# Performance work log

Hardware: AMD Instinct MI355X
Metric: run time of the kernel (lower is better)

Reference implementation:

```python
import jax, jax.numpy as jnp
import numpy as np

EPS = 1e-12      # F.normalize eps
LN_EPS = 1e-5    # nn.LayerNorm eps
SLOPE = 0.01     # LeakyReLU negative slope
SCALE = 5.0      # attention temperature used by the module


def _l2norm(x):
    n = jnp.sqrt(jnp.sum(x * x, axis=-1, keepdims=True))
    return x / jnp.maximum(n, EPS)


def _layer_norm(x, g, b):
    m = jnp.mean(x, axis=-1, keepdims=True)
    v = jnp.mean((x - m) ** 2, axis=-1, keepdims=True)
    return (x - m) / jnp.sqrt(v + LN_EPS) * g + b


def _leaky(x):
    return jnp.where(x >= 0, x, SLOPE * x)


def setup_inputs() -> dict:
    key = jax.random.key(0)
    ks = jax.random.split(key, 18)
    B, T, N, C = 8, 8, 25, 256
    n = T * N  # 200 == num_nodes
    inp = {
        "local_feat": jax.random.normal(ks[0], (B, T, N, C), dtype=jnp.float32),
        "global_feat": jax.random.normal(ks[1], (B, C), dtype=jnp.float32),
        "pos": jax.random.uniform(ks[2], (B, T, N, 9), dtype=jnp.float32),
        # Diff_prop params
        "dp_adj_w": jax.random.normal(ks[3], (C, C), dtype=jnp.float32) / np.sqrt(C),
        "dp_aff_w": jax.random.normal(ks[4], (C, C), dtype=jnp.float32) * np.sqrt(2.0 / C),
        "dp_aff_b": jnp.zeros((C,), dtype=jnp.float32),
        "dp_ln_g": jnp.ones((C,), dtype=jnp.float32),
        "dp_ln_b": jnp.zeros((C,), dtype=jnp.float32),
        # Feat_aggr params
        "fa_adj_w": jax.random.normal(ks[5], (C, C), dtype=jnp.float32) / np.sqrt(C),
        "fa_aff_w": jax.random.normal(ks[6], (C, C), dtype=jnp.float32) * np.sqrt(2.0 / C),
        "fa_aff_b": jnp.zeros((C,), dtype=jnp.float32),
        "fa_ln_g": jnp.ones((C,), dtype=jnp.float32),
        "fa_ln_b": jnp.zeros((C,), dtype=jnp.float32),
        # Node_att params (Linear(num_nodes+9, 1): weight [1, n+9])
        "na_w": jax.random.normal(ks[7], (1, n + 9), dtype=jnp.float32) * np.sqrt(2.0 / (n + 9)),
        "na_b": jnp.zeros((1,), dtype=jnp.float32),
    }
    return inp


def _diff_prop(lf4, adj_w, aff_w, aff_b, ln_g, ln_b):
    B, T, N, C = lf4.shape
    n = T * N
    lf = lf4.reshape(B, n, C)
    nf = _l2norm(lf)
    # quadratic-form attention: A[b,i,j] = nf_i W nf_j
    A = jnp.einsum('bnc,cd,bmd->bnm', nf, adj_w, nf)
    A = jnp.exp(SCALE * (A - jnp.max(A, axis=-1, keepdims=True)))
    A = A * (1.0 - jnp.eye(n, dtype=A.dtype))
    A = A / jnp.maximum(jnp.sum(A, axis=-1, keepdims=True), EPS)  # L1 row norm (A>=0)
    # full pairwise difference tensor [B, n, n, C]
    diff = lf[:, :, None, :] - lf[:, None, :, :]
    diff = jnp.einsum('bijc,dc->bijd', diff, aff_w) + aff_b
    agg = jnp.einsum('bij,bijd->bid', A, diff)
    out = _leaky(_layer_norm(agg, ln_g, ln_b))
    return out.reshape(B, T, N, C)


def _feat_aggr(lf4, adj_w, aff_w, aff_b, ln_g, ln_b):
    B, T, N, C = lf4.shape
    n = T * N
    lf = lf4.reshape(B, n, C)
    nf = _l2norm(lf)
    A = jnp.einsum('bnc,cd,bmd->bnm', nf, adj_w, nf)
    A = jax.nn.softmax(SCALE * (A - jnp.max(A, axis=-1, keepdims=True)), axis=-1)
    lf = jnp.einsum('bnc,dc->bnd', lf, aff_w) + aff_b
    lf = jnp.einsum('bij,bjk->bik', A, lf)
    out = _leaky(_layer_norm(lf, ln_g, ln_b))
    return out.reshape(B, T, N, C)


def _node_att(lf4, pos, w, b):
    B, T, N, C = lf4.shape
    n = T * N
    lf = lf4.reshape(B, n, C)
    p = pos.reshape(B, n, -1)
    nf = _l2norm(lf)
    A = jnp.einsum('bnc,bmc->bnm', nf, nf)            # [B, n, n]
    src = jnp.concatenate([A, p], axis=-1)            # [B, n, n+9]
    att = jax.nn.sigmoid(jnp.einsum('bni,oi->bno', src, w) + b)  # [B, n, 1]
    att = att.reshape(B, T, N, 1)
    return lf4 * att


def reference(local_feat, global_feat, pos,
              dp_adj_w, dp_aff_w, dp_aff_b, dp_ln_g, dp_ln_b,
              fa_adj_w, fa_aff_w, fa_aff_b, fa_ln_g, fa_ln_b,
              na_w, na_b):
    x = _diff_prop(local_feat, dp_adj_w, dp_aff_w, dp_aff_b, dp_ln_g, dp_ln_b)
    x = _feat_aggr(x, fa_adj_w, fa_aff_w, fa_aff_b, fa_ln_g, fa_ln_b)
    x = _node_att(x, pos, na_w, na_b)
    return x
```

## Files before the change

kernel.cpp:

```cpp
#include <hip/hip_runtime.h>
#include <math.h>

#define Bn 8
#define NN 200
#define Cc 256
#define RR (Bn*NN)
#define JP 200
#define N_EPS 1e-12f
#define LN_EPS 1e-5f
#define SLOPE 0.01f
#define SCALE 5.0f

#define FMA4(acc, s, v) { acc.x = fmaf((s), (v).x, acc.x); acc.y = fmaf((s), (v).y, acc.y); \
                          acc.z = fmaf((s), (v).z, acc.z); acc.w = fmaf((s), (v).w, acc.w); }

__device__ __forceinline__ float wave_reduce_sum(float v) {
    #pragma unroll
    for (int o = 32; o > 0; o >>= 1) v += __shfl_xor(v, o);
    return v;
}

__device__ __forceinline__ float2 half_reduce_sum2(float2 v, float* sh, int h) {
    __syncthreads();
    #pragma unroll
    for (int o = 32; o > 0; o >>= 1) { v.x += __shfl_xor(v.x, o); v.y += __shfl_xor(v.y, o); }
    int w = threadIdx.x >> 6;
    if ((threadIdx.x & 63) == 0) { sh[w*2] = v.x; sh[w*2+1] = v.y; }
    __syncthreads();
    int b0 = h * 8;
    return make_float2(sh[b0]+sh[b0+2]+sh[b0+4]+sh[b0+6],
                       sh[b0+1]+sh[b0+3]+sh[b0+5]+sh[b0+7]);
}

__device__ __forceinline__ float2 half_reduce_max2(float2 v, float* sh, int h) {
    __syncthreads();
    #pragma unroll
    for (int o = 32; o > 0; o >>= 1) {
        v.x = fmaxf(v.x, __shfl_xor(v.x, o));
        v.y = fmaxf(v.y, __shfl_xor(v.y, o));
    }
    int w = threadIdx.x >> 6;
    if ((threadIdx.x & 63) == 0) { sh[w*2] = v.x; sh[w*2+1] = v.y; }
    __syncthreads();
    int b0 = h * 8;
    return make_float2(fmaxf(fmaxf(sh[b0],sh[b0+2]), fmaxf(sh[b0+4],sh[b0+6])),
                       fmaxf(fmaxf(sh[b0+1],sh[b0+3]), fmaxf(sh[b0+5],sh[b0+7])));
}

__global__ void k_tr(const float* __restrict__ dp_aff_w, const float* __restrict__ fa_aff_w,
                     float* __restrict__ WT1, float* __restrict__ WT2) {
    __shared__ float tile[32][33];
    int tb = blockIdx.x;
    const float* S; float* D;
    if (tb < 64) { S = dp_aff_w; D = WT1; } else { S = fa_aff_w; D = WT2; tb -= 64; }
    int bx = tb & 7, by = tb >> 3;
    int tx = threadIdx.x & 31, ty = threadIdx.x >> 5;
    #pragma unroll
    for (int k = 0; k < 32; k += 8)
        tile[ty + k][tx] = S[(size_t)(by*32 + ty + k) * Cc + bx*32 + tx];
    __syncthreads();
    #pragma unroll
    for (int k = 0; k < 32; k += 8)
        D[(size_t)(bx*32 + ty + k) * Cc + by*32 + tx] = tile[tx][ty + k];
}

__global__ void k_pre(const float* __restrict__ lf, const float* __restrict__ dp_adj_w,
                      const float* __restrict__ WT1,
                      float* __restrict__ nfT, float* __restrict__ M, float* __restrict__ P) {
    __shared__ __align__(16) float sx[8][Cc];
    __shared__ __align__(16) float buf[8192];
    int bid = blockIdx.x;
    int t = threadIdx.x, lane = t & 63, wvi = t >> 6;
    bool nb = bid < RR/8;
    int r0 = (nb ? bid : bid - RR/8) * 8;
    const float* W = nb ? dp_adj_w : WT1;
    #pragma unroll
    for (int k = 0; k < 2; k++) {
        int r = 2*wvi + k;
        float4 x = ((const float4*)(lf + (size_t)(r0 + r) * Cc))[lane];
        if (nb) {
            float ss = wave_reduce_sum(x.x*x.x + x.y*x.y + x.z*x.z + x.w*x.w);
            float inv = 1.f / fmaxf(sqrtf(ss), N_EPS);
            x.x *= inv; x.y *= inv; x.z *= inv; x.w *= inv;
        }
        ((float4*)&sx[r][0])[lane] = x;
    }
    __syncthreads();
    if (nb) {
        int b = r0 / NN, i0 = r0 % NN;
        float4 cA, cB;
        cA.x = sx[0][t]; cA.y = sx[1][t]; cA.z = sx[2][t]; cA.w = sx[3][t];
        cB.x = sx[4][t]; cB.y = sx[5][t]; cB.z = sx[6][t]; cB.w = sx[7][t];
        float* np = nfT + (size_t)b * Cc * JP + (size_t)t * JP + i0;
        *((float4*)np) = cA;
        *((float4*)(np + 4)) = cB;
    }
    {
        int qc = t & 63, cid = t >> 6;
        int c0 = cid * 64;
        float4 z = make_float4(0.f,0.f,0.f,0.f);
        float4 acc0=z, acc1=z, acc2=z, acc3=z, acc4=z, acc5=z, acc6=z, acc7=z;
        #pragma unroll 4
        for (int c4 = c0; c4 < c0 + 64; c4 += 4) {
            float4 w0 = *(const float4*)(W + (size_t)(c4+0) * Cc + 4*qc);
            float4 w1 = *(const float4*)(W + (size_t)(c4+1) * Cc + 4*qc);
            float4 w2 = *(const float4*)(W + (size_t)(c4+2) * Cc + 4*qc);
            float4 w3 = *(const float4*)(W + (size_t)(c4+3) * Cc + 4*qc);
            float4 xr;
            xr = *(const float4*)(&sx[0][c4]);
            FMA4(acc0, xr.x, w0); FMA4(acc0, xr.y, w1); FMA4(acc0, xr.z, w2); FMA4(acc0, xr.w, w3);
            xr = *(const float4*)(&sx[1][c4]);
            FMA4(acc1, xr.x, w0); FMA4(acc1, xr.y, w1); FMA4(acc1, xr.z, w2); FMA4(acc1, xr.w, w3);
            xr = *(const float4*)(&sx[2][c4]);
            FMA4(acc2, xr.x, w0); FMA4(acc2, xr.y, w1); FMA4(acc2, xr.z, w2); FMA4(acc2, xr.w, w3);
            xr = *(const float4*)(&sx[3][c4]);
            FMA4(acc3, xr.x, w0); FMA4(acc3, xr.y, w1); FMA4(acc3, xr.z, w2); FMA4(acc3, xr.w, w3);
            xr = *(const float4*)(&sx[4][c4]);
            FMA4(acc4, xr.x, w0); FMA4(acc4, xr.y, w1); FMA4(acc4, xr.z, w2); FMA4(acc4, xr.w, w3);
            xr = *(const float4*)(&sx[5][c4]);
            FMA4(acc5, xr.x, w0); FMA4(acc5, xr.y, w1); FMA4(acc5, xr.z, w2); FMA4(acc5, xr.w, w3);
            xr = *(const float4*)(&sx[6][c4]);
            FMA4(acc6, xr.x, w0); FMA4(acc6, xr.y, w1); FMA4(acc6, xr.z, w2); FMA4(acc6, xr.w, w3);
            xr = *(const float4*)(&sx[7][c4]);
            FMA4(acc7, xr.x, w0); FMA4(acc7, xr.y, w1); FMA4(acc7, xr.z, w2); FMA4(acc7, xr.w, w3);
        }
        float4* b4 = (float4*)buf;
        int o = cid * 512 + qc;
        b4[o      ] = acc0; b4[o +  64] = acc1; b4[o + 128] = acc2; b4[o + 192] = acc3;
        b4[o + 256] = acc4; b4[o + 320] = acc5; b4[o + 384] = acc6; b4[o + 448] = acc7;
    }
    __syncthreads();
    {
        float4* b4 = (float4*)buf;
        float* Y = nb ? M : P;
        #pragma unroll
        for (int k = 0; k < 2; k++) {
            int o4 = t + k*256;
            int r = o4 >> 6, qc = o4 & 63;
            float4 s0 = b4[o4], s1 = b4[512 + o4], s2 = b4[1024 + o4], s3 = b4[1536 + o4];
            float4 sv;
            sv.x = (s0.x + s1.x) + (s2.x + s3.x);
            sv.y = (s0.y + s1.y) + (s2.y + s3.y);
            sv.z = (s0.z + s1.z) + (s2.z + s3.z);
            sv.w = (s0.w + s1.w) + (s2.w + s3.w);
            *(float4*)(Y + (size_t)(r0 + r) * Cc + 4*qc) = sv;
        }
    }
}

__global__ void k_row1f(const float* __restrict__ nfT, const float* __restrict__ Min,
                        const float* __restrict__ P, const float* __restrict__ dp_aff_b,
                        const float* __restrict__ g, const float* __restrict__ bb,
                        const float* __restrict__ fa_adj_w, const float* __restrict__ WT2,
                        const float* __restrict__ fa_aff_b,
                        float* __restrict__ nfT2, float* __restrict__ M2,
                        float* __restrict__ lf2) {
    __shared__ __align__(16) float smT[Cc*4];
    __shared__ __align__(16) float saraw[4*NN];
    __shared__ __align__(16) float saT[NN*4];
    __shared__ __align__(16) float suT[Cc*4];
    __shared__ __align__(16) float buf[8192];
    __shared__ float sh[16];
    __shared__ float sinv[4];
    int t = threadIdx.x, h = t >> 8, tt = t & 255;
    int b = blockIdx.x & 7;
    int i0 = (blockIdx.x >> 3) * 4;
    size_t base = (size_t)b * NN * Cc;
    {
        const float* src = Min + base + (size_t)i0 * Cc;
        #pragma unroll
        for (int o = t; o < 1024; o += 512) {
            int c = o >> 2, r = o & 3;
            smT[o] = src[(size_t)r * Cc + c];
        }
    }
    __syncthreads();
    {
        int q = t & 63, cid = t >> 6;
        if (q < 50) {
            int c0 = cid * 32;
            const float* nfp = nfT + (size_t)b * Cc * JP + (size_t)c0 * JP + 4*q;
            float4 z4 = make_float4(0.f,0.f,0.f,0.f);
            float4 a0 = z4, a1 = z4, a2 = z4, a3 = z4;
            #pragma unroll 8
            for (int c = 0; c < 32; c++) {
                float4 v  = *(const float4*)(nfp + (size_t)c * JP);
                float4 mv = *(const float4*)(&smT[(c0 + c) * 4]);
                FMA4(a0, mv.x, v); FMA4(a1, mv.y, v);
                FMA4(a2, mv.z, v); FMA4(a3, mv.w, v);
            }
            float* pp = buf + cid * 800 + 4*q;
            *(float4*)(pp      ) = a0;
            *(float4*)(pp + 200) = a1;
            *(float4*)(pp + 400) = a2;
            *(float4*)(pp + 600) = a3;
        }
    }
    __syncthreads();
    for (int o = t; o < 800; o += 512) {
        float s = 0.f;
        #pragma unroll
        for (int p = 0; p < 8; p++) s += buf[p*800 + o];
        saraw[o] = s;
    }
    __syncthreads();
    int lr0 = h, lr1 = h + 2;
    float2 vm;
    vm.x = (tt < NN) ? saraw[lr0*NN + tt] : -INFINITY;
    vm.y = (tt < NN) ? saraw[lr1*NN + tt] : -INFINITY;
    float2 m = half_reduce_max2(vm, sh, h);
    float e0 = (tt < NN && tt != i0 + lr0) ? expf(SCALE * (vm.x - m.x)) : 0.f;
    float e1 = (tt < NN && tt != i0 + lr1) ? expf(SCALE * (vm.y - m.y)) : 0.f;
    float2 sum = half_reduce_sum2(make_float2(e0, e1), sh, h);
    if (tt < NN) {
        saT[tt*4 + lr0] = e0 / fmaxf(sum.x, N_EPS);
        saT[tt*4 + lr1] = e1 / fmaxf(sum.y, N_EPS);
    }
    float s0 = sum.x / fmaxf(sum.x, N_EPS);
    float s1 = sum.y / fmaxf(sum.y, N_EPS);
    __syncthreads();
    const float* Pb = P + base;
    {
        int qc = t & 63, jc = t >> 6;
        int j0 = jc * 25;
        float4 z4 = make_float4(0.f,0.f,0.f,0.f);
        float4 u0 = z4, u1 = z4, u2 = z4, u3 = z4;
        #pragma unroll 5
        for (int j = j0; j < j0 + 25; j++) {
            float4 pv = *(const float4*)(Pb + (size_t)j * Cc + 4*qc);
            float4 av = *(const float4*)(&saT[j*4]);
            FMA4(u0, av.x, pv); FMA4(u1, av.y, pv);
            FMA4(u2, av.z, pv); FMA4(u3, av.w, pv);
        }
        float* pp = buf + jc*1024 + 4*qc;
        *(float4*)(pp      ) = u0;
        *(float4*)(pp + 256) = u1;
        *(float4*)(pp + 512) = u2;
        *(float4*)(pp + 768) = u3;
    }
    __syncthreads();
    float acc0 = 0.f, acc1 = 0.f;
    #pragma unroll
    for (int p = 0; p < 8; p++) { acc0 += buf[p*1024 + t]; acc1 += buf[p*1024 + t + 512]; }
    float bv = dp_aff_b[tt];
    float y0 = fmaf(s0, Pb[(size_t)(i0 + lr0) * Cc + tt] + bv, -acc0);
    float y1 = fmaf(s1, Pb[(size_t)(i0 + lr1) * Cc + tt] + bv, -acc1);
    float gg = g[tt], bbv = bb[tt];
    float2 mean2 = half_reduce_sum2(make_float2(y0, y1), sh, h);
    float d0 = y0 - mean2.x * (1.f/256.f);
    float d1 = y1 - mean2.y * (1.f/256.f);
    float2 var2 = half_reduce_sum2(make_float2(d0*d0, d1*d1), sh, h);
    float z0 = d0 / sqrtf(var2.x * (1.f/256.f) + LN_EPS) * gg + bbv;
    float z1 = d1 / sqrtf(var2.y * (1.f/256.f) + LN_EPS) * gg + bbv;
    z0 = (z0 >= 0.f) ? z0 : SLOPE * z0;
    z1 = (z1 >= 0.f) ? z1 : SLOPE * z1;
    suT[tt*4 + lr0] = z0; suT[tt*4 + lr1] = z1;
    float2 ss2 = half_reduce_sum2(make_float2(z0*z0, z1*z1), sh, h);
    if (tt == 0) {
        sinv[lr0] = 1.f / fmaxf(sqrtf(ss2.x), N_EPS);
        sinv[lr1] = 1.f / fmaxf(sqrtf(ss2.y), N_EPS);
    }
    __syncthreads();
    if (h == 0) {
        float4 col;
        col.x = suT[tt*4+0] * sinv[0]; col.y = suT[tt*4+1] * sinv[1];
        col.z = suT[tt*4+2] * sinv[2]; col.w = suT[tt*4+3] * sinv[3];
        *((float4*)(nfT2 + (size_t)b * Cc * JP + (size_t)tt * JP + i0)) = col;
    }
    {
        int qc = t & 63, gidx = t >> 6;
        int mt = gidx & 1, cch = gidx >> 1;
        const float* Wm = mt ? WT2 : fa_adj_w;
        int c0 = cch * 64;
        float4 z4 = make_float4(0.f,0.f,0.f,0.f);
        float4 d0v = z4, d1v = z4, d2v = z4, d3v = z4;
        #pragma unroll 8
        for (int c = c0; c < c0 + 64; c++) {
            float4 wv = *(const float4*)(Wm + (size_t)c * Cc + 4*qc);
            float4 uv = *(const float4*)(&suT[c*4]);
            FMA4(d0v, uv.x, wv); FMA4(d1v, uv.y, wv);
            FMA4(d2v, uv.z, wv); FMA4(d3v, uv.w, wv);
        }
        float* pp = buf + cch*2048 + mt*1024 + 4*qc;
        *(float4*)(pp      ) = d0v;
        *(float4*)(pp + 256) = d1v;
        *(float4*)(pp + 512) = d2v;
        *(float4*)(pp + 768) = d3v;
    }
    __syncthreads();
    {
        float4* b4 = (float4*)buf;
        int o4 = t;
        int mt2 = o4 >> 8, r2 = (o4 >> 6) & 3, qc2 = o4 & 63;
        float4 s0 = b4[o4], s1 = b4[512 + o4], s2 = b4[1024 + o4], s3 = b4[1536 + o4];
        float4 sv;
        sv.x = (s0.x + s1.x) + (s2.x + s3.x);
        sv.y = (s0.y + s1.y) + (s2.y + s3.y);
        sv.z = (s0.z + s1.z) + (s2.z + s3.z);
        sv.w = (s0.w + s1.w) + (s2.w + s3.w);
        if (mt2 == 0) {
            float sc = sinv[r2];
            sv.x *= sc; sv.y *= sc; sv.z *= sc; sv.w *= sc;
            *(float4*)(M2 + base + (size_t)(i0 + r2) * Cc + 4*qc2) = sv;
        } else {
            float4 fb = *(const float4*)(fa_aff_b + 4*qc2);
            sv.x += fb.x; sv.y += fb.y; sv.z += fb.z; sv.w += fb.w;
            *(float4*)(lf2 + base + (size_t)(i0 + r2) * Cc + 4*qc2) = sv;
        }
    }
}

__global__ void k_row2f(const float* __restrict__ nfT2, const float* __restrict__ M2,
                        const float* __restrict__ lf2, const float* __restrict__ g,
                        const float* __restrict__ bb, float* __restrict__ x2,
                        float* __restrict__ nf3) {
    __shared__ __align__(16) float smT[Cc*4];
    __shared__ __align__(16) float saraw[4*NN];
    __shared__ __align__(16) float saT[NN*4];
    __shared__ __align__(16) float buf[8192];
    __shared__ float sh[16];
    int t = threadIdx.x, h = t >> 8, tt = t & 255;
    int b = blockIdx.x & 7;
    int i0 = (blockIdx.x >> 3) * 4;
    size_t base = (size_t)b * NN * Cc;
    {
        const float* src = M2 + base + (size_t)i0 * Cc;
        #pragma unroll
        for (int o = t; o < 1024; o += 512) {
            int c = o >> 2, r = o & 3;
            smT[o] = src[(size_t)r * Cc + c];
        }
    }
    __syncthreads();
    {
        int q = t & 63, cid = t >> 6;
        if (q < 50) {
            int c0 = cid * 32;
            const float* nfp = nfT2 + (size_t)b * Cc * JP + (size_t)c0 * JP + 4*q;
            float4 z4 = make_float4(0.f,0.f,0.f,0.f);
            float4 a0 = z4, a1 = z4, a2 = z4, a3 = z4;
            #pragma unroll 8
            for (int c = 0; c < 32; c++) {
                float4 v  = *(const float4*)(nfp + (size_t)c * JP);
                float4 mv = *(const float4*)(&smT[(c0 + c) * 4]);
                FMA4(a0, mv.x, v); FMA4(a1, mv.y, v);
                FMA4(a2, mv.z, v); FMA4(a3, mv.w, v);
            }
            float* pp = buf + cid * 800 + 4*q;
            *(float4*)(pp      ) = a0;
            *(float4*)(pp + 200) = a1;
            *(float4*)(pp + 400) = a2;
            *(float4*)(pp + 600) = a3;
        }
    }
    __syncthreads();
    for (int o = t; o < 800; o += 512) {
        float s = 0.f;
        #pragma unroll
        for (int p = 0; p < 8; p++) s += buf[p*800 + o];
        saraw[o] = s;
    }
    __syncthreads();
    int lr0 = h, lr1 = h + 2;
    float2 vm;
    vm.x = (tt < NN) ? saraw[lr0*NN + tt] : -INFINITY;
    vm.y = (tt < NN) ? saraw[lr1*NN + tt] : -INFINITY;
    float2 m = half_reduce_max2(vm, sh, h);
    float e0 = (tt < NN) ? expf(SCALE * (vm.x - m.x)) : 0.f;
    float e1 = (tt < NN) ? expf(SCALE * (vm.y - m.y)) : 0.f;
    float2 sum = half_reduce_sum2(make_float2(e0, e1), sh, h);
    if (tt < NN) { saT[tt*4 + lr0] = e0 / sum.x; saT[tt*4 + lr1] = e1 / sum.y; }
    __syncthreads();
    const float* l2b = lf2 + base;
    {
        int qc = t & 63, jc = t >> 6;
        int j0 = jc * 25;
        float4 z4 = make_float4(0.f,0.f,0.f,0.f);
        float4 u0 = z4, u1 = z4, u2 = z4, u3 = z4;
        #pragma unroll 5
        for (int j = j0; j < j0 + 25; j++) {
            float4 pv = *(const float4*)(l2b + (size_t)j * Cc + 4*qc);
            float4 av = *(const float4*)(&saT[j*4]);
            FMA4(u0, av.x, pv); FMA4(u1, av.y, pv);
            FMA4(u2, av.z, pv); FMA4(u3, av.w, pv);
        }
        float* pp = buf + jc*1024 + 4*qc;
        *(float4*)(pp      ) = u0;
        *(float4*)(pp + 256) = u1;
        *(float4*)(pp + 512) = u2;
        *(float4*)(pp + 768) = u3;
    }
    __syncthreads();
    float y0 = 0.f, y1 = 0.f;
    #pragma unroll
    for (int p = 0; p < 8; p++) { y0 += buf[p*1024 + t]; y1 += buf[p*1024 + t + 512]; }
    float gg = g[tt], bbv = bb[tt];
    float2 mean2 = half_reduce_sum2(make_float2(y0, y1), sh, h);
    float d0 = y0 - mean2.x * (1.f/256.f);
    float d1 = y1 - mean2.y * (1.f/256.f);
    float2 var2 = half_reduce_sum2(make_float2(d0*d0, d1*d1), sh, h);
    float z0 = d0 / sqrtf(var2.x * (1.f/256.f) + LN_EPS) * gg + bbv;
    float z1 = d1 / sqrtf(var2.y * (1.f/256.f) + LN_EPS) * gg + bbv;
    z0 = (z0 >= 0.f) ? z0 : SLOPE * z0;
    z1 = (z1 >= 0.f) ? z1 : SLOPE * z1;
    x2[base + (size_t)(i0 + lr0) * Cc + tt] = z0;
    x2[base + (size_t)(i0 + lr1) * Cc + tt] = z1;
    float2 ss2 = half_reduce_sum2(make_float2(z0*z0, z1*z1), sh, h);
    nf3[base + (size_t)(i0 + lr0) * Cc + tt] = z0 / fmaxf(sqrtf(ss2.x), N_EPS);
    nf3[base + (size_t)(i0 + lr1) * Cc + tt] = z1 / fmaxf(sqrtf(ss2.y), N_EPS);
}

__global__ void k_natt(const float* __restrict__ x2, const float* __restrict__ nf3,
                       const float* __restrict__ pos, const float* __restrict__ w,
                       const float* __restrict__ nb, float* __restrict__ out) {
    __shared__ float svb[4][Cc];
    int t = threadIdx.x, lane = t & 63, wv = t >> 6;
    int b = blockIdx.x & 7;
    int i = (blockIdx.x >> 3) * 4 + wv;
    const float4* slab = (const float4*)(nf3 + (size_t)b * NN * Cc);
    float4 acc = make_float4(0.f, 0.f, 0.f, 0.f);
    for (int j = wv * 50; j < wv * 50 + 50; j++) {
        float4 q = slab[j * 64 + lane];
        float wj = w[j];
        acc.x = fmaf(wj, q.x, acc.x);
        acc.y = fmaf(wj, q.y, acc.y);
        acc.z = fmaf(wj, q.z, acc.z);
        acc.w = fmaf(wj, q.w, acc.w);
    }
    ((float4*)&svb[wv][0])[lane] = acc;
    __syncthreads();
    float4 p0 = ((const float4*)&svb[0][0])[lane];
    float4 p1 = ((const float4*)&svb[1][0])[lane];
    float4 p2 = ((const float4*)&svb[2][0])[lane];
    float4 p3 = ((const float4*)&svb[3][0])[lane];
    float4 vb;
    vb.x = (p0.x + p1.x) + (p2.x + p3.x);
    vb.y = (p0.y + p1.y) + (p2.y + p3.y);
    vb.z = (p0.z + p1.z) + (p2.z + p3.z);
    vb.w = (p0.w + p1.w) + (p2.w + p3.w);
    size_t bi = (size_t)b * NN + i;
    float4 nv = ((const float4*)(nf3 + bi * Cc))[lane];
    float val = nv.x*vb.x + nv.y*vb.y + nv.z*vb.z + nv.w*vb.w;
    if (lane < 9) val += pos[bi * 9 + lane] * w[NN + lane];
    val = wave_reduce_sum(val);
    float att = 1.f / (1.f + expf(-(val + nb[0])));
    float4 xo = ((const float4*)(x2 + bi * Cc))[lane];
    xo.x *= att; xo.y *= att; xo.z *= att; xo.w *= att;
    ((float4*)(out + bi * Cc))[lane] = xo;
}

extern "C" void kernel_launch(void* const* d_in, const int* in_sizes, int n_in,
                              void* d_out, int out_size, void* d_ws, size_t ws_size,
                              hipStream_t stream) {
    (void)in_sizes; (void)n_in; (void)out_size; (void)ws_size;
    const float* lf       = (const float*)d_in[0];
    const float* pos      = (const float*)d_in[2];
    const float* dp_adj_w = (const float*)d_in[3];
    const float* dp_aff_w = (const float*)d_in[4];
    const float* dp_aff_b = (const float*)d_in[5];
    const float* dp_ln_g  = (const float*)d_in[6];
    const float* dp_ln_b  = (const float*)d_in[7];
    const float* fa_adj_w = (const float*)d_in[8];
    const float* fa_aff_w = (const float*)d_in[9];
    const float* fa_aff_b = (const float*)d_in[10];
    const float* fa_ln_g  = (const float*)d_in[11];
    const float* fa_ln_b  = (const float*)d_in[12];
    const float* na_w     = (const float*)d_in[13];
    const float* na_b     = (const float*)d_in[14];
    float* out = (float*)d_out;
    float* ws  = (float*)d_ws;

    float* nfT  = ws;
    float* nfT2 = nfT  + Bn * Cc * JP;
    float* M    = nfT2 + Bn * Cc * JP;
    float* P    = M    + RR * Cc;
    float* lf2  = P    + RR * Cc;
    float* x2   = lf2  + RR * Cc;
    float* nf3  = x2   + RR * Cc;
    float* WT1  = nf3  + RR * Cc;
    float* WT2  = WT1  + Cc * Cc;

    k_tr   <<<128,        dim3(256), 0, stream>>>(dp_aff_w, fa_aff_w, WT1, WT2);
    k_pre  <<<RR/8 * 2,   dim3(256), 0, stream>>>(lf, dp_adj_w, WT1, nfT, M, P);
    k_row1f<<<Bn * NN/4,  dim3(512), 0, stream>>>(nfT, M, P, dp_aff_b, dp_ln_g, dp_ln_b,
                                                  fa_adj_w, WT2, fa_aff_b, nfT2, M, lf2);
    k_row2f<<<Bn * NN/4,  dim3(512), 0, stream>>>(nfT2, M, lf2, fa_ln_g, fa_ln_b, x2, nf3);
    k_natt <<<Bn * NN/4,  dim3(256), 0, stream>>>(x2, nf3, pos, na_w, na_b, out);
}
```

Baseline: 64.20 us.

## Reassociate affine projection after attention aggregation and fold transpose into pre kernel

Instead of precomputing P = lf·W^T for all rows in k_pre, k_row1f now aggregates raw lf with the attention weights and applies WT1 to the 4-row result afterwards, using (A·lf)·W^T = A·(lf·W^T). The separate transpose kernel is merged into k_pre as extra blocks, which removes one launch and drops the P buffer write and read. In exchange, k_row1f gains an extra 256x256 matvec per block with more synchronisation, and WT1 is read repeatedly by 400 blocks.

```diff
diff --git a/kernel.cpp b/kernel.cpp
--- a/kernel.cpp
+++ b/kernel.cpp
@@ -47,65 +47,46 @@
                        fmaxf(fmaxf(sh[b0+1],sh[b0+3]), fmaxf(sh[b0+5],sh[b0+7])));
 }
 
-__global__ void k_tr(const float* __restrict__ dp_aff_w, const float* __restrict__ fa_aff_w,
-                     float* __restrict__ WT1, float* __restrict__ WT2) {
-    __shared__ float tile[32][33];
-    int tb = blockIdx.x;
-    const float* S; float* D;
-    if (tb < 64) { S = dp_aff_w; D = WT1; } else { S = fa_aff_w; D = WT2; tb -= 64; }
-    int bx = tb & 7, by = tb >> 3;
-    int tx = threadIdx.x & 31, ty = threadIdx.x >> 5;
-    #pragma unroll
-    for (int k = 0; k < 32; k += 8)
-        tile[ty + k][tx] = S[(size_t)(by*32 + ty + k) * Cc + bx*32 + tx];
-    __syncthreads();
-    #pragma unroll
-    for (int k = 0; k < 32; k += 8)
-        D[(size_t)(bx*32 + ty + k) * Cc + by*32 + tx] = tile[tx][ty + k];
-}
-
 __global__ void k_pre(const float* __restrict__ lf, const float* __restrict__ dp_adj_w,
-                      const float* __restrict__ WT1,
-                      float* __restrict__ nfT, float* __restrict__ M, float* __restrict__ P) {
+                      const float* __restrict__ dp_aff_w, const float* __restrict__ fa_aff_w,
+                      float* __restrict__ nfT, float* __restrict__ M,
+                      float* __restrict__ WT1, float* __restrict__ WT2) {
     __shared__ __align__(16) float sx[8][Cc];
     __shared__ __align__(16) float buf[8192];
+    __shared__ float tile[32][33];
     int bid = blockIdx.x;
     int t = threadIdx.x, lane = t & 63, wvi = t >> 6;
-    bool nb = bid < RR/8;
-    int r0 = (nb ? bid : bid - RR/8) * 8;
-    const float* W = nb ? dp_adj_w : WT1;
-    #pragma unroll
-    for (int k = 0; k < 2; k++) {
-        int r = 2*wvi + k;
-        float4 x = ((const float4*)(lf + (size_t)(r0 + r) * Cc))[lane];
-        if (nb) {
+    if (bid < RR/8) {
+        int r0 = bid * 8;
+        #pragma unroll
+        for (int k = 0; k < 2; k++) {
+            int r = 2*wvi + k;
+            float4 x = ((const float4*)(lf + (size_t)(r0 + r) * Cc))[lane];
             float ss = wave_reduce_sum(x.x*x.x + x.y*x.y + x.z*x.z + x.w*x.w);
             float inv = 1.f / fmaxf(sqrtf(ss), N_EPS);
             x.x *= inv; x.y *= inv; x.z *= inv; x.w *= inv;
-        }
-        ((float4*)&sx[r][0])[lane] = x;
-    }
-    __syncthreads();
-    if (nb) {
-        int b = r0 / NN, i0 = r0 % NN;
-        float4 cA, cB;
-        cA.x = sx[0][t]; cA.y = sx[1][t]; cA.z = sx[2][t]; cA.w = sx[3][t];
-        cB.x = sx[4][t]; cB.y = sx[5][t]; cB.z = sx[6][t]; cB.w = sx[7][t];
-        float* np = nfT + (size_t)b * Cc * JP + (size_t)t * JP + i0;
-        *((float4*)np) = cA;
-        *((float4*)(np + 4)) = cB;
-    }
-    {
+            ((float4*)&sx[r][0])[lane] = x;
+        }
+        __syncthreads();
+        {
+            int b = r0 / NN, i0 = r0 % NN;
+            float4 cA, cB;
+            cA.x = sx[0][t]; cA.y = sx[1][t]; cA.z = sx[2][t]; cA.w = sx[3][t];
+            cB.x = sx[4][t]; cB.y = sx[5][t]; cB.z = sx[6][t]; cB.w = sx[7][t];
+            float* np = nfT + (size_t)b * Cc * JP + (size_t)t * JP + i0;
+            *((float4*)np) = cA;
+            *((float4*)(np + 4)) = cB;
+        }
         int qc = t & 63, cid = t >> 6;
         int c0 = cid * 64;
         float4 z = make_float4(0.f,0.f,0.f,0.f);
         float4 acc0=z, acc1=z, acc2=z, acc3=z, acc4=z, acc5=z, acc6=z, acc7=z;
         #pragma unroll 4
         for (int c4 = c0; c4 < c0 + 64; c4 += 4) {
-            float4 w0 = *(const float4*)(W + (size_t)(c4+0) * Cc + 4*qc);
-            float4 w1 = *(const float4*)(W + (size_t)(c4+1) * Cc + 4*qc);
-            float4 w2 = *(const float4*)(W + (size_t)(c4+2) * Cc + 4*qc);
-            float4 w3 = *(const float4*)(W + (size_t)(c4+3) * Cc + 4*qc);
+            float4 w0 = *(const float4*)(dp_adj_w + (size_t)(c4+0) * Cc + 4*qc);
+            float4 w1 = *(const float4*)(dp_adj_w + (size_t)(c4+1) * Cc + 4*qc);
+            float4 w2 = *(const float4*)(dp_adj_w + (size_t)(c4+2) * Cc + 4*qc);
+            float4 w3 = *(const float4*)(dp_adj_w + (size_t)(c4+3) * Cc + 4*qc);
             float4 xr;
             xr = *(const float4*)(&sx[0][c4]);
             FMA4(acc0, xr.x, w0); FMA4(acc0, xr.y, w1); FMA4(acc0, xr.z, w2); FMA4(acc0, xr.w, w3);
@@ -128,28 +109,38 @@
         int o = cid * 512 + qc;
         b4[o      ] = acc0; b4[o +  64] = acc1; b4[o + 128] = acc2; b4[o + 192] = acc3;
         b4[o + 256] = acc4; b4[o + 320] = acc5; b4[o + 384] = acc6; b4[o + 448] = acc7;
-    }
-    __syncthreads();
-    {
-        float4* b4 = (float4*)buf;
-        float* Y = nb ? M : P;
+        __syncthreads();
         #pragma unroll
         for (int k = 0; k < 2; k++) {
             int o4 = t + k*256;
-            int r = o4 >> 6, qc = o4 & 63;
+            int r = o4 >> 6, qc2 = o4 & 63;
             float4 s0 = b4[o4], s1 = b4[512 + o4], s2 = b4[1024 + o4], s3 = b4[1536 + o4];
             float4 sv;
             sv.x = (s0.x + s1.x) + (s2.x + s3.x);
             sv.y = (s0.y + s1.y) + (s2.y + s3.y);
             sv.z = (s0.z + s1.z) + (s2.z + s3.z);
             sv.w = (s0.w + s1.w) + (s2.w + s3.w);
-            *(float4*)(Y + (size_t)(r0 + r) * Cc + 4*qc) = sv;
-        }
+            *(float4*)(M + (size_t)(r0 + r) * Cc + 4*qc2) = sv;
+        }
+    } else {
+        int tb = bid - RR/8;
+        const float* S; float* D;
+        if (tb < 64) { S = dp_aff_w; D = WT1; } else { S = fa_aff_w; D = WT2; tb -= 64; }
+        int bx = tb & 7, by = tb >> 3;
+        int tx = t & 31, ty = t >> 5;
+        #pragma unroll
+        for (int k = 0; k < 32; k += 8)
+            tile[ty + k][tx] = S[(size_t)(by*32 + ty + k) * Cc + bx*32 + tx];
+        __syncthreads();
+        #pragma unroll
+        for (int k = 0; k < 32; k += 8)
+            D[(size_t)(bx*32 + ty + k) * Cc + by*32 + tx] = tile[tx][ty + k];
     }
 }
 
 __global__ void k_row1f(const float* __restrict__ nfT, const float* __restrict__ Min,
-                        const float* __restrict__ P, const float* __restrict__ dp_aff_b,
+                        const float* __restrict__ lf, const float* __restrict__ dp_aff_b,
+                        const float* __restrict__ WT1,
                         const float* __restrict__ g, const float* __restrict__ bb,
                         const float* __restrict__ fa_adj_w, const float* __restrict__ WT2,
                         const float* __restrict__ fa_aff_b,
@@ -219,7 +210,7 @@
     float s0 = sum.x / fmaxf(sum.x, N_EPS);
     float s1 = sum.y / fmaxf(sum.y, N_EPS);
     __syncthreads();
-    const float* Pb = P + base;
+    const float* lfb = lf + base;
     {
         int qc = t & 63, jc = t >> 6;
         int j0 = jc * 25;
@@ -227,7 +218,7 @@
         float4 u0 = z4, u1 = z4, u2 = z4, u3 = z4;
         #pragma unroll 5
         for (int j = j0; j < j0 + 25; j++) {
-            float4 pv = *(const float4*)(Pb + (size_t)j * Cc + 4*qc);
+            float4 pv = *(const float4*)(lfb + (size_t)j * Cc + 4*qc);
             float4 av = *(const float4*)(&saT[j*4]);
             FMA4(u0, av.x, pv); FMA4(u1, av.y, pv);
             FMA4(u2, av.z, pv); FMA4(u3, av.w, pv);
@@ -242,9 +233,37 @@
     float acc0 = 0.f, acc1 = 0.f;
     #pragma unroll
     for (int p = 0; p < 8; p++) { acc0 += buf[p*1024 + t]; acc1 += buf[p*1024 + t + 512]; }
+    float U0 = fmaf(s0, lfb[(size_t)(i0 + lr0) * Cc + tt], -acc0);
+    float U1 = fmaf(s1, lfb[(size_t)(i0 + lr1) * Cc + tt], -acc1);
+    __syncthreads();
+    smT[tt*4 + lr0] = U0;
+    smT[tt*4 + lr1] = U1;
+    __syncthreads();
+    {
+        int qc = t & 63, cid = t >> 6;
+        int c0 = cid * 32;
+        float4 z4 = make_float4(0.f,0.f,0.f,0.f);
+        float4 p0 = z4, p1 = z4, p2 = z4, p3 = z4;
+        #pragma unroll 8
+        for (int c = c0; c < c0 + 32; c++) {
+            float4 wv = *(const float4*)(WT1 + (size_t)c * Cc + 4*qc);
+            float4 uv = *(const float4*)(&smT[c*4]);
+            FMA4(p0, uv.x, wv); FMA4(p1, uv.y, wv);
+            FMA4(p2, uv.z, wv); FMA4(p3, uv.w, wv);
+        }
+        float* pp = buf + cid*1024 + 4*qc;
+        *(float4*)(pp      ) = p0;
+        *(float4*)(pp + 256) = p1;
+        *(float4*)(pp + 512) = p2;
+        *(float4*)(pp + 768) = p3;
+    }
+    __syncthreads();
+    float y0 = 0.f, y1 = 0.f;
+    #pragma unroll
+    for (int p = 0; p < 8; p++) { y0 += buf[p*1024 + t]; y1 += buf[p*1024 + t + 512]; }
     float bv = dp_aff_b[tt];
-    float y0 = fmaf(s0, Pb[(size_t)(i0 + lr0) * Cc + tt] + bv, -acc0);
-    float y1 = fmaf(s1, Pb[(size_t)(i0 + lr1) * Cc + tt] + bv, -acc1);
+    y0 += s0 * bv;
+    y1 += s1 * bv;
     float gg = g[tt], bbv = bb[tt];
     float2 mean2 = half_reduce_sum2(make_float2(y0, y1), sh, h);
     float d0 = y0 - mean2.x * (1.f/256.f);
@@ -292,12 +311,12 @@
         float4* b4 = (float4*)buf;
         int o4 = t;
         int mt2 = o4 >> 8, r2 = (o4 >> 6) & 3, qc2 = o4 & 63;
-        float4 s0 = b4[o4], s1 = b4[512 + o4], s2 = b4[1024 + o4], s3 = b4[1536 + o4];
+        float4 v0 = b4[o4], v1 = b4[512 + o4], v2 = b4[1024 + o4], v3 = b4[1536 + o4];
         float4 sv;
-        sv.x = (s0.x + s1.x) + (s2.x + s3.x);
-        sv.y = (s0.y + s1.y) + (s2.y + s3.y);
-        sv.z = (s0.z + s1.z) + (s2.z + s3.z);
-        sv.w = (s0.w + s1.w) + (s2.w + s3.w);
+        sv.x = (v0.x + v1.x) + (v2.x + v3.x);
+        sv.y = (v0.y + v1.y) + (v2.y + v3.y);
+        sv.z = (v0.z + v1.z) + (v2.z + v3.z);
+        sv.w = (v0.w + v1.w) + (v2.w + v3.w);
         if (mt2 == 0) {
             float sc = sinv[r2];
             sv.x *= sc; sv.y *= sc; sv.z *= sc; sv.w *= sc;
@@ -473,17 +492,17 @@
     float* nfT  = ws;
     float* nfT2 = nfT  + Bn * Cc * JP;
     float* M    = nfT2 + Bn * Cc * JP;
-    float* P    = M    + RR * Cc;
-    float* lf2  = P    + RR * Cc;
+    float* lf2  = M    + RR * Cc;
     float* x2   = lf2  + RR * Cc;
     float* nf3  = x2   + RR * Cc;
     float* WT1  = nf3  + RR * Cc;
     float* WT2  = WT1  + Cc * Cc;
 
-    k_tr   <<<128,        dim3(256), 0, stream>>>(dp_aff_w, fa_aff_w, WT1, WT2);
-    k_pre  <<<RR/8 * 2,   dim3(256), 0, stream>>>(lf, dp_adj_w, WT1, nfT, M, P);
-    k_row1f<<<Bn * NN/4,  dim3(512), 0, stream>>>(nfT, M, P, dp_aff_b, dp_ln_g, dp_ln_b,
-                                                  fa_adj_w, WT2, fa_aff_b, nfT2, M, lf2);
+    k_pre  <<<RR/8 + 128, dim3(256), 0, stream>>>(lf, dp_adj_w, dp_aff_w, fa_aff_w,
+                                                  nfT, M, WT1, WT2);
+    k_row1f<<<Bn * NN/4,  dim3(512), 0, stream>>>(nfT, M, lf, dp_aff_b, WT1,
+                                                  dp_ln_g, dp_ln_b, fa_adj_w, WT2, fa_aff_b,
+                                                  nfT2, M, lf2);
     k_row2f<<<Bn * NN/4,  dim3(512), 0, stream>>>(nfT2, M, lf2, fa_ln_g, fa_ln_b, x2, nf3);
     k_natt <<<Bn * NN/4,  dim3(256), 0, stream>>>(x2, nf3, pos, na_w, na_b, out);
 }
```

Result: faster. 61.73 us (median of 2 runs) (-3.9%).
